# Kernel tuning notes

Measured on AMD Instinct MI355X. Metric: run time of the kernel, lower is better.

Reference implementation:

```python
import jax, jax.numpy as jnp
import numpy as np

D_MODEL = 512
NUM_HEADS = 8
HEAD_DIM = D_MODEL // NUM_HEADS
WINDOW = 64


def setup_inputs() -> dict:
    key = jax.random.key(0)
    ks = jax.random.split(key, 9)
    B, L = 4, 2048
    s = 1.0 / np.sqrt(D_MODEL)
    return {
        "x": jax.random.normal(ks[0], (B, L, D_MODEL), dtype=jnp.float32),
        "Wq": jax.random.normal(ks[1], (D_MODEL, D_MODEL), dtype=jnp.float32) * s,
        "bq": jnp.zeros((D_MODEL,), jnp.float32),
        "Wk": jax.random.normal(ks[2], (D_MODEL, D_MODEL), dtype=jnp.float32) * s,
        "bk": jnp.zeros((D_MODEL,), jnp.float32),
        "Wv": jax.random.normal(ks[3], (D_MODEL, D_MODEL), dtype=jnp.float32) * s,
        "bv": jnp.zeros((D_MODEL,), jnp.float32),
        "Wo": jax.random.normal(ks[4], (D_MODEL, D_MODEL), dtype=jnp.float32) * s,
        "bo": jnp.zeros((D_MODEL,), jnp.float32),
    }


def reference(x, Wq, bq, Wk, bk, Wv, bv, Wo, bo):
    B, L, _ = x.shape
    # projections -> [B, H, L, Dh]
    def proj(W, b):
        return (x @ W + b).reshape(B, L, NUM_HEADS, HEAD_DIM).transpose(0, 2, 1, 3)
    q, k, v = proj(Wq, bq), proj(Wk, bk), proj(Wv, bv)
    scores = jnp.einsum("bhqd,bhkd->bhqk", q, k) / np.sqrt(HEAD_DIM)
    idx = jnp.arange(L)
    dist = jnp.abs(idx[None, :] - idx[:, None])  # [L, L]
    mask = dist > WINDOW
    scores = jnp.where(mask[None, None], -jnp.inf, scores)
    attn = jax.nn.softmax(scores, axis=-1)  # dropout p inert in eval
    out = jnp.einsum("bhqk,bhkd->bhqd", attn, v)
    out = out.transpose(0, 2, 1, 3).reshape(B, L, D_MODEL)
    return out @ Wo + bo
```

## Files before the change

kernel.cpp:

```cpp
#include <hip/hip_runtime.h>
#include <cstdint>
#include <cstddef>

typedef _Float16 f16;
typedef f16 f16x8 __attribute__((ext_vector_type(8)));
typedef f16 f16x4 __attribute__((ext_vector_type(4)));
typedef float floatx4 __attribute__((ext_vector_type(4)));

#define GAS __attribute__((address_space(1)))
#define LAS __attribute__((address_space(3)))

static constexpr int LSEQ = 2048;
static constexpr int NH   = 8;
static constexpr int DH   = 64;
static constexpr int DM   = 512;
static constexpr int WIN  = 64;
static constexpr int MR   = 4 * LSEQ;

__global__ __launch_bounds__(256) void cast_x_kernel(const float* __restrict__ x,
                                                     f16* __restrict__ xb) {
    int i = blockIdx.x * 256 + threadIdx.x;
    float4 v = ((const float4*)x)[i];
    f16x4 o = { (f16)v.x, (f16)v.y, (f16)v.z, (f16)v.w };
    ((f16x4*)xb)[i] = o;
}

__global__ void wt_kernel(const float* __restrict__ Wq, const float* __restrict__ Wk,
                          const float* __restrict__ Wv, const float* __restrict__ Wo,
                          f16* __restrict__ wt) {
    __shared__ float tile[32][33];
    int z = blockIdx.z;
    const float* W = z == 0 ? Wq : z == 1 ? Wk : z == 2 ? Wv : Wo;
    f16* out = wt + (size_t)z * DM * DM;
    int c0 = blockIdx.x * 32, r0 = blockIdx.y * 32;
    int tx = threadIdx.x, ty = threadIdx.y;
    #pragma unroll
    for (int i = 0; i < 32; i += 8)
        tile[ty + i][tx] = W[(size_t)(r0 + ty + i) * DM + c0 + tx];
    __syncthreads();
    #pragma unroll
    for (int i = 0; i < 32; i += 8)
        out[(size_t)(c0 + ty + i) * DM + r0 + tx] = (f16)tile[tx][ty + i];
}

template <bool QKV>
__global__ __launch_bounds__(256) void gemm_kernel(
    const f16* __restrict__ A, const f16* __restrict__ Bt_base,
    const float* __restrict__ b0, const float* __restrict__ b1,
    const float* __restrict__ b2,
    f16* __restrict__ out_q, f16* __restrict__ out_k, f16* __restrict__ out_vt,
    float* __restrict__ out_f) {
    const int z = QKV ? blockIdx.z : 0;
    const f16* __restrict__ Bt = Bt_base + (size_t)z * (DM * DM);
    const float* __restrict__ bias = QKV ? (z == 0 ? b0 : z == 1 ? b1 : b2) : b0;

    __shared__ f16 As[128 * 64];
    __shared__ f16 Bs[128 * 64];

    const int tid  = threadIdx.x;
    const int wid  = tid >> 6;
    const int lane = tid & 63;
    const int l15  = lane & 15;
    const int l4   = lane >> 4;
    const int m0   = blockIdx.y * 128;
    const int n0   = blockIdx.x * 128;
    const int wr   = wid >> 1, wc = wid & 1;

    floatx4 acc[4][4] = {};

    for (int k0 = 0; k0 < DM; k0 += 64) {
        #pragma unroll
        for (int i = 0; i < 4; ++i) {
            int c   = i * 256 + wid * 64 + lane;
            int row = c >> 3, cw = c & 7;
            int cs  = cw ^ (row & 7);
            const f16* ga = A  + (size_t)(m0 + row) * DM + k0 + cs * 8;
            const f16* gb = Bt + (size_t)(n0 + row) * DM + k0 + cs * 8;
            f16* la = &As[(i * 256 + wid * 64) * 8];
            f16* lb = &Bs[(i * 256 + wid * 64) * 8];
            __builtin_amdgcn_global_load_lds((const GAS void*)ga, (LAS void*)la, 16, 0, 0);
            __builtin_amdgcn_global_load_lds((const GAS void*)gb, (LAS void*)lb, 16, 0, 0);
        }
        __syncthreads();
        #pragma unroll
        for (int ks = 0; ks < 2; ++ks) {
            f16x8 af[4], bfr[4];
            #pragma unroll
            for (int m = 0; m < 4; ++m) {
                int row = wr * 64 + m * 16 + l15;
                int kc  = (ks * 4 + l4) ^ (row & 7);
                af[m] = *(const f16x8*)(&As[row * 64 + kc * 8]);
            }
            #pragma unroll
            for (int n = 0; n < 4; ++n) {
                int row = wc * 64 + n * 16 + l15;
                int kc  = (ks * 4 + l4) ^ (row & 7);
                bfr[n] = *(const f16x8*)(&Bs[row * 64 + kc * 8]);
            }
            #pragma unroll
            for (int m = 0; m < 4; ++m)
                #pragma unroll
                for (int n = 0; n < 4; ++n)
                    acc[m][n] = __builtin_amdgcn_mfma_f32_16x16x32_f16(af[m], bfr[n], acc[m][n], 0, 0, 0);
        }
        __syncthreads();
    }

    #pragma unroll
    for (int n = 0; n < 4; ++n) {
        int gcol = n0 + wc * 64 + n * 16 + l15;
        float bias_v = bias[gcol];
        #pragma unroll
        for (int m = 0; m < 4; ++m) {
            int grow0 = m0 + wr * 64 + m * 16 + l4 * 4;
            #pragma unroll
            for (int r = 0; r < 4; ++r) {
                int grow = grow0 + r;
                float v = acc[m][n][r] + bias_v;
                if constexpr (QKV) {
                    int b = grow >> 11, lp = grow & (LSEQ - 1);
                    int h = gcol >> 6,  d  = gcol & (DH - 1);
                    int bh = b * NH + h;
                    if (z == 0)
                        out_q[((size_t)bh * LSEQ + lp) * DH + d] = (f16)(v * 0.125f);
                    else if (z == 1)
                        out_k[((size_t)bh * LSEQ + lp) * DH + d] = (f16)v;
                    else
                        out_vt[((size_t)bh * DH + d) * LSEQ + lp] = (f16)v;
                } else {
                    out_f[(size_t)grow * DM + gcol] = v;
                }
            }
        }
    }
}

__global__ __launch_bounds__(256) void attn_kernel(const f16* __restrict__ Qb,
                                                   const f16* __restrict__ Kb,
                                                   const f16* __restrict__ Vt,
                                                   f16* __restrict__ Ob) {
    const int bh     = blockIdx.y;
    const int q0blk  = blockIdx.x * 64;
    const int wid    = threadIdx.x >> 6;
    const int lane   = threadIdx.x & 63;
    const int l15    = lane & 15, l4 = lane >> 4;
    const int qbase  = q0blk + wid * 16;
    const int kstart = q0blk - WIN;

    const f16* __restrict__ Q = Qb + (size_t)bh * LSEQ * DH;
    const f16* __restrict__ K = Kb + (size_t)bh * LSEQ * DH;
    const f16* __restrict__ V = Vt + (size_t)bh * DH * LSEQ;

    __shared__ f16 Pl[4][16][232];

    f16x8 qf[2];
    #pragma unroll
    for (int ks = 0; ks < 2; ++ks)
        qf[ks] = *(const f16x8*)(Q + (size_t)(qbase + l15) * DH + ks * 32 + l4 * 8);

    floatx4 sc[12] = {};
    #pragma unroll
    for (int nt = 0; nt < 12; ++nt) {
        int key = kstart + nt * 16 + l15;
        int kcl = key < 0 ? 0 : (key > LSEQ - 1 ? LSEQ - 1 : key);
        #pragma unroll
        for (int ks = 0; ks < 2; ++ks) {
            f16x8 kf = *(const f16x8*)(K + (size_t)kcl * DH + ks * 32 + l4 * 8);
            sc[nt] = __builtin_amdgcn_mfma_f32_16x16x32_f16(qf[ks], kf, sc[nt], 0, 0, 0);
        }
    }

    float mx[4] = {-1e30f, -1e30f, -1e30f, -1e30f};
    #pragma unroll
    for (int nt = 0; nt < 12; ++nt) {
        int key = kstart + nt * 16 + l15;
        #pragma unroll
        for (int r = 0; r < 4; ++r) {
            int q = qbase + l4 * 4 + r;
            int dist = key - q; dist = dist < 0 ? -dist : dist;
            bool valid = (key >= 0) && (key < LSEQ) && (dist <= WIN);
            float s = valid ? sc[nt][r] : -1e30f;
            sc[nt][r] = s;
            mx[r] = fmaxf(mx[r], s);
        }
    }
    #pragma unroll
    for (int r = 0; r < 4; ++r)
        #pragma unroll
        for (int m = 1; m < 16; m <<= 1)
            mx[r] = fmaxf(mx[r], __shfl_xor(mx[r], m, 64));
    float sm[4] = {0.f, 0.f, 0.f, 0.f};
    #pragma unroll
    for (int nt = 0; nt < 12; ++nt)
        #pragma unroll
        for (int r = 0; r < 4; ++r) {
            float p = __expf(sc[nt][r] - mx[r]);
            sc[nt][r] = p;
            sm[r] += p;
        }
    #pragma unroll
    for (int r = 0; r < 4; ++r) {
        #pragma unroll
        for (int m = 1; m < 16; m <<= 1)
            sm[r] += __shfl_xor(sm[r], m, 64);
        sm[r] = 1.f / sm[r];
    }

    #pragma unroll
    for (int nt = 0; nt < 12; ++nt)
        #pragma unroll
        for (int r = 0; r < 4; ++r)
            Pl[wid][l4 * 4 + r][nt * 16 + l15] = (f16)(sc[nt][r] * sm[r]);
    __syncthreads();

    floatx4 oc[4] = {};
    #pragma unroll
    for (int ks = 0; ks < 6; ++ks) {
        f16x8 pf = *(const f16x8*)(&Pl[wid][l15][ks * 32 + l4 * 8]);
        int kb0 = kstart + ks * 32 + l4 * 8;
        int kbc = (kb0 < 0 || kb0 > LSEQ - 8) ? 0 : kb0;
        #pragma unroll
        for (int dt = 0; dt < 4; ++dt) {
            f16x8 vf = *(const f16x8*)(V + (size_t)(dt * 16 + l15) * LSEQ + kbc);
            oc[dt] = __builtin_amdgcn_mfma_f32_16x16x32_f16(pf, vf, oc[dt], 0, 0, 0);
        }
    }

    int b = bh >> 3, h = bh & 7;
    #pragma unroll
    for (int dt = 0; dt < 4; ++dt) {
        int d = dt * 16 + l15;
        #pragma unroll
        for (int r = 0; r < 4; ++r) {
            int q = qbase + l4 * 4 + r;
            Ob[((size_t)b * LSEQ + q) * DM + h * DH + d] = (f16)oc[dt][r];
        }
    }
}

extern "C" void kernel_launch(void* const* d_in, const int* in_sizes, int n_in,
                              void* d_out, int out_size, void* d_ws, size_t ws_size,
                              hipStream_t stream) {
    const float* x  = (const float*)d_in[0];
    const float* Wq = (const float*)d_in[1];
    const float* bq = (const float*)d_in[2];
    const float* Wk = (const float*)d_in[3];
    const float* bk = (const float*)d_in[4];
    const float* Wv = (const float*)d_in[5];
    const float* bv = (const float*)d_in[6];
    const float* Wo = (const float*)d_in[7];
    const float* bo = (const float*)d_in[8];
    float* out = (float*)d_out;

    char* ws = (char*)d_ws;
    f16* xb = (f16*)(ws);
    f16* wt = (f16*)(ws + (8ull << 20));
    f16* qb = (f16*)(ws + (10ull << 20));
    f16* kb = (f16*)(ws + (18ull << 20));
    f16* vt = (f16*)(ws + (26ull << 20));
    f16* ob = (f16*)(ws + (34ull << 20));

    cast_x_kernel<<<dim3(MR * DM / 4 / 256), 256, 0, stream>>>(x, xb);
    wt_kernel<<<dim3(16, 16, 4), dim3(32, 8), 0, stream>>>(Wq, Wk, Wv, Wo, wt);
    gemm_kernel<true><<<dim3(4, 64, 3), 256, 0, stream>>>(
        xb, wt, bq, bk, bv, qb, kb, vt, nullptr);
    attn_kernel<<<dim3(LSEQ / 64, 32), 256, 0, stream>>>(qb, kb, vt, ob);
    gemm_kernel<false><<<dim3(4, 64, 1), 256, 0, stream>>>(
        ob, wt + 3ull * DM * DM, bo, bo, bo, nullptr, nullptr, nullptr, out);
}
```

Baseline: 93.03 us.

## Double-buffer GEMM LDS tiles to overlap global loads with MFMA compute

Splits the GEMM shared-memory A/B tiles into two buffers. The global-to-LDS load of the next K slice is issued before the MFMA work on the current slice, which removes one barrier per iteration and hides load latency. The K loop is fully unrolled, and the launch bound now requests two blocks per CU. LDS use doubles to 64KB per block, which may limit occupancy. The single remaining barrier per step has to cover both the RAW and WAR hazards on the async LDS loads.

```diff
diff --git a/kernel.cpp b/kernel.cpp
--- a/kernel.cpp
+++ b/kernel.cpp
@@ -44,7 +44,7 @@
 }
 
 template <bool QKV>
-__global__ __launch_bounds__(256) void gemm_kernel(
+__global__ __launch_bounds__(256, 2) void gemm_kernel(
     const f16* __restrict__ A, const f16* __restrict__ Bt_base,
     const float* __restrict__ b0, const float* __restrict__ b1,
     const float* __restrict__ b2,
@@ -54,8 +54,8 @@
     const f16* __restrict__ Bt = Bt_base + (size_t)z * (DM * DM);
     const float* __restrict__ bias = QKV ? (z == 0 ? b0 : z == 1 ? b1 : b2) : b0;
 
-    __shared__ f16 As[128 * 64];
-    __shared__ f16 Bs[128 * 64];
+    __shared__ f16 As[2][128 * 64];
+    __shared__ f16 Bs[2][128 * 64];
 
     const int tid  = threadIdx.x;
     const int wid  = tid >> 6;
@@ -68,20 +68,25 @@
 
     floatx4 acc[4][4] = {};
 
-    for (int k0 = 0; k0 < DM; k0 += 64) {
+    int c_     = wid * 64 + lane;
+    int row_   = c_ >> 3, cw_ = c_ & 7;
+    int cs_    = cw_ ^ (row_ & 7);
+
+    auto stage = [&](int buf, int k0) {
         #pragma unroll
         for (int i = 0; i < 4; ++i) {
-            int c   = i * 256 + wid * 64 + lane;
-            int row = c >> 3, cw = c & 7;
-            int cs  = cw ^ (row & 7);
+            int row = row_ + i * 32;
+            int cs  = cw_ ^ (row & 7);
             const f16* ga = A  + (size_t)(m0 + row) * DM + k0 + cs * 8;
             const f16* gb = Bt + (size_t)(n0 + row) * DM + k0 + cs * 8;
-            f16* la = &As[(i * 256 + wid * 64) * 8];
-            f16* lb = &Bs[(i * 256 + wid * 64) * 8];
+            f16* la = &As[buf][(i * 256 + wid * 64 + lane) * 8 - lane * 8 + lane * 8];
+            la = &As[buf][(i * 256 + wid * 64) * 8];
+            f16* lb = &Bs[buf][(i * 256 + wid * 64) * 8];
             __builtin_amdgcn_global_load_lds((const GAS void*)ga, (LAS void*)la, 16, 0, 0);
             __builtin_amdgcn_global_load_lds((const GAS void*)gb, (LAS void*)lb, 16, 0, 0);
         }
-        __syncthreads();
+    };
+    auto compute = [&](int buf) {
         #pragma unroll
         for (int ks = 0; ks < 2; ++ks) {
             f16x8 af[4], bfr[4];
@@ -89,13 +94,13 @@
             for (int m = 0; m < 4; ++m) {
                 int row = wr * 64 + m * 16 + l15;
                 int kc  = (ks * 4 + l4) ^ (row & 7);
-                af[m] = *(const f16x8*)(&As[row * 64 + kc * 8]);
+                af[m] = *(const f16x8*)(&As[buf][row * 64 + kc * 8]);
             }
             #pragma unroll
             for (int n = 0; n < 4; ++n) {
                 int row = wc * 64 + n * 16 + l15;
                 int kc  = (ks * 4 + l4) ^ (row & 7);
-                bfr[n] = *(const f16x8*)(&Bs[row * 64 + kc * 8]);
+                bfr[n] = *(const f16x8*)(&Bs[buf][row * 64 + kc * 8]);
             }
             #pragma unroll
             for (int m = 0; m < 4; ++m)
@@ -103,7 +108,15 @@
                 for (int n = 0; n < 4; ++n)
                     acc[m][n] = __builtin_amdgcn_mfma_f32_16x16x32_f16(af[m], bfr[n], acc[m][n], 0, 0, 0);
         }
-        __syncthreads();
+    };
+
+    stage(0, 0);
+    __syncthreads();
+    #pragma unroll
+    for (int t = 0; t < 8; ++t) {
+        if (t < 7) stage((t + 1) & 1, (t + 1) * 64);
+        compute(t & 1);
+        if (t < 7) __syncthreads();
     }
 
     #pragma unroll
```

New measurement: 86.76 us. -6.7%, faster.

## Double-buffer GEMM K-loop with 128-wide chunks and manual vmcnt waits

Applied to the files above, without the earlier changes.

Replaces the 8-iteration K loop with 64-wide tiles by a fully unrolled schedule over four 128-wide K chunks held in two LDS buffers. The next chunk's global-to-LDS loads are issued before computing the current one, with explicit vmcnt waits and barriers. The goal is to overlap memory latency with MFMA work and halve the number of barriers. LDS use rises to 128KB per block and launch bounds pin occupancy to one block per CU, so latency hiding now depends entirely on the software pipeline.

```diff
diff --git a/kernel.cpp b/kernel.cpp
--- a/kernel.cpp
+++ b/kernel.cpp
@@ -44,7 +44,7 @@
 }
 
 template <bool QKV>
-__global__ __launch_bounds__(256) void gemm_kernel(
+__global__ __launch_bounds__(256, 1) void gemm_kernel(
     const f16* __restrict__ A, const f16* __restrict__ Bt_base,
     const float* __restrict__ b0, const float* __restrict__ b1,
     const float* __restrict__ b2,
@@ -54,8 +54,8 @@
     const f16* __restrict__ Bt = Bt_base + (size_t)z * (DM * DM);
     const float* __restrict__ bias = QKV ? (z == 0 ? b0 : z == 1 ? b1 : b2) : b0;
 
-    __shared__ f16 As[128 * 64];
-    __shared__ f16 Bs[128 * 64];
+    __shared__ f16 As[2 * 128 * 128];
+    __shared__ f16 Bs[2 * 128 * 128];
 
     const int tid  = threadIdx.x;
     const int wid  = tid >> 6;
@@ -68,34 +68,32 @@
 
     floatx4 acc[4][4] = {};
 
-    for (int k0 = 0; k0 < DM; k0 += 64) {
-        #pragma unroll
-        for (int i = 0; i < 4; ++i) {
-            int c   = i * 256 + wid * 64 + lane;
-            int row = c >> 3, cw = c & 7;
-            int cs  = cw ^ (row & 7);
-            const f16* ga = A  + (size_t)(m0 + row) * DM + k0 + cs * 8;
-            const f16* gb = Bt + (size_t)(n0 + row) * DM + k0 + cs * 8;
-            f16* la = &As[(i * 256 + wid * 64) * 8];
-            f16* lb = &Bs[(i * 256 + wid * 64) * 8];
-            __builtin_amdgcn_global_load_lds((const GAS void*)ga, (LAS void*)la, 16, 0, 0);
-            __builtin_amdgcn_global_load_lds((const GAS void*)gb, (LAS void*)lb, 16, 0, 0);
-        }
-        __syncthreads();
-        #pragma unroll
-        for (int ks = 0; ks < 2; ++ks) {
+    auto stage = [&](const f16* __restrict__ src, f16* lds, int r0, int k0, int half) {
+        #pragma unroll
+        for (int i = 0; i < 8; ++i) {
+            int q   = i * 256 + tid;
+            int row = q >> 4, ci = q & 15;
+            int cis = ci ^ (row & 7);
+            const f16* g = src + (size_t)(r0 + row) * DM + k0 + half * 128 + cis * 8;
+            f16* l = lds + half * 16384 + (i * 256 + wid * 64) * 8;
+            __builtin_amdgcn_global_load_lds((const GAS void*)g, (LAS void*)l, 16, 0, 0);
+        }
+    };
+    auto compute_half = [&](int half) {
+        #pragma unroll
+        for (int ks = 0; ks < 4; ++ks) {
             f16x8 af[4], bfr[4];
             #pragma unroll
             for (int m = 0; m < 4; ++m) {
                 int row = wr * 64 + m * 16 + l15;
-                int kc  = (ks * 4 + l4) ^ (row & 7);
-                af[m] = *(const f16x8*)(&As[row * 64 + kc * 8]);
+                int cis = (ks * 4 + l4) ^ (row & 7);
+                af[m] = *(const f16x8*)(&As[half * 16384 + row * 128 + cis * 8]);
             }
             #pragma unroll
             for (int n = 0; n < 4; ++n) {
                 int row = wc * 64 + n * 16 + l15;
-                int kc  = (ks * 4 + l4) ^ (row & 7);
-                bfr[n] = *(const f16x8*)(&Bs[row * 64 + kc * 8]);
+                int cis = (ks * 4 + l4) ^ (row & 7);
+                bfr[n] = *(const f16x8*)(&Bs[half * 16384 + row * 128 + cis * 8]);
             }
             #pragma unroll
             for (int m = 0; m < 4; ++m)
@@ -103,8 +101,31 @@
                 for (int n = 0; n < 4; ++n)
                     acc[m][n] = __builtin_amdgcn_mfma_f32_16x16x32_f16(af[m], bfr[n], acc[m][n], 0, 0, 0);
         }
-        __syncthreads();
-    }
+    };
+    auto wait_bar = [&](int n) {
+        if (n == 16) asm volatile("s_waitcnt vmcnt(16)" ::: "memory");
+        else         asm volatile("s_waitcnt vmcnt(0)" ::: "memory");
+        __builtin_amdgcn_sched_barrier(0);
+        __builtin_amdgcn_s_barrier();
+        __builtin_amdgcn_sched_barrier(0);
+    };
+
+    stage(A, As, m0, 0, 0);  stage(Bt, Bs, n0, 0, 0);
+    stage(A, As, m0, 0, 1);  stage(Bt, Bs, n0, 0, 1);
+    wait_bar(16);
+    compute_half(0);
+    __builtin_amdgcn_s_barrier();
+    __builtin_amdgcn_sched_barrier(0);
+    stage(A, As, m0, 256, 0); stage(Bt, Bs, n0, 256, 0);
+    wait_bar(16);
+    compute_half(1);
+    __builtin_amdgcn_s_barrier();
+    __builtin_amdgcn_sched_barrier(0);
+    stage(A, As, m0, 256, 1); stage(Bt, Bs, n0, 256, 1);
+    wait_bar(16);
+    compute_half(0);
+    wait_bar(0);
+    compute_half(1);
 
     #pragma unroll
     for (int n = 0; n < 4; ++n) {
```

Result: no change. 94.04 us (+1.1%).
